# Kernel tuning notes

Hardware: AMD Instinct MI355X
Metric: run time of the kernel (lower is better)

Reference implementation:

```python
import jax, jax.numpy as jnp
import numpy as np

T_DIL = 10   # neighbor-count threshold
K_DIL = 2    # skip hyperparameter
BN_EPS = 1e-5
NORM_EPS = 1e-12


def _dilate_pattern(adj_bool, mask_b):
    """Sequential (row-by-row) dilated neighbor skipping on a [N,N] bool adjacency.
    Faithful to the torch double loop: earlier rows' removals (including the
    symmetric column zeroing) affect later rows' neighbor sets."""
    N = adj_bool.shape[0]

    def step(carry, n):
        row = jnp.take(carry, n, axis=0)                 # [N] bool, current neighbors of n
        nbi = row.astype(jnp.int32)
        num = jnp.sum(nbi)
        sf = jnp.where(num > T_DIL, (num + K_DIL - 1) // K_DIL, 1)  # linear mode, ceil(num/k)
        rank = jnp.cumsum(nbi)                           # 1-based rank among neighbors
        rm = row & ((rank % sf) == 0)                    # neighbors[sf-1::sf]
        valid = (mask_b[n] != 0) & (num > 1)
        rm = jnp.where(valid, rm, False)
        keep = ~rm
        carry = carry.at[n].set(row & keep)              # adj[n, to_remove] = 0
        carry = carry.at[:, n].set(carry[:, n] & keep)   # adj[to_remove, n] = 0
        return carry, None

    out, _ = jax.lax.scan(step, adj_bool, jnp.arange(N))
    return out


def _dilate(adj, mask):
    # keep-pattern is piecewise constant in adj; multiply so removed entries -> 0
    keep = jax.vmap(_dilate_pattern)(adj > 0, mask)
    return adj * keep.astype(adj.dtype)


def _sage(x, adj, Wr, Wx, b, mf):
    # DenseSAGEConv: mean-aggregate, lin_rel + lin_root, L2 normalize, mask
    deg = jnp.clip(jnp.sum(adj, axis=-1, keepdims=True), 1.0, None)
    agg = jnp.einsum('bij,bjd->bid', adj, x) / deg
    out = agg @ Wr + x @ Wx + b
    nrm = jnp.maximum(jnp.linalg.norm(out, axis=-1, keepdims=True), NORM_EPS)
    return (out / nrm) * mf[..., None]


def _bn(x, g, b):
    # BatchNorm1d in training mode over flattened (B*N) rows, biased variance
    m = jnp.mean(x, axis=(0, 1))
    v = jnp.var(x, axis=(0, 1))
    return (x - m) * jax.lax.rsqrt(v + BN_EPS) * g + b


def _forward(x, adj, mask, Wr1, Wx1, b1, g1, be1, Wr2, Wx2, b2, g2, be2,
             Wr3, Wx3, b3, g3, be3, Wl, bl):
    mf = mask.astype(x.dtype)
    # linear dilation mode: skip factor is layer-independent, and each layer
    # dilates the ORIGINAL adj (torch clones adj per call) -> compute once
    adj_d = _dilate(adj, mask)
    h1 = _bn(jax.nn.relu(_sage(x, adj_d, Wr1, Wx1, b1, mf)), g1, be1)
    h2 = _bn(jax.nn.relu(_sage(h1, adj_d, Wr2, Wx2, b2, mf)), g2, be2)
    h3 = _bn(jax.nn.relu(_sage(h2, adj_d, Wr3, Wx3, b3, mf)), g3, be3)
    xc = jnp.concatenate([h1, h2, h3], axis=-1) * mf[..., None]
    return (xc @ Wl + bl) * mf[..., None]


def setup_inputs() -> dict:
    B, N, D, H, E = 8, 2048, 128, 128, 128
    key = jax.random.key(0)
    ks = jax.random.split(key, 24)
    x = jax.random.normal(ks[0], (B, N, D), dtype=jnp.float32)
    a = jax.random.bernoulli(ks[1], 0.01, (B, N, N))
    a = a | jnp.swapaxes(a, 1, 2)
    a = a & ~jnp.eye(N, dtype=bool)[None]
    adj = a.astype(jnp.float32)
    mask = jnp.ones((B, N), dtype=jnp.int32)
    s = 0.05
    p = {}
    dims = [(D, H), (H, H), (H, E)]
    for i, (di, do) in enumerate(dims, 1):
        p[f'Wr{i}'] = s * jax.random.normal(ks[2 * i], (di, do), dtype=jnp.float32)
        p[f'Wx{i}'] = s * jax.random.normal(ks[2 * i + 1], (di, do), dtype=jnp.float32)
        p[f'b{i}'] = jnp.zeros((do,), dtype=jnp.float32)
        p[f'g{i}'] = jnp.ones((do,), dtype=jnp.float32)
        p[f'be{i}'] = jnp.zeros((do,), dtype=jnp.float32)
    p['Wl'] = s * jax.random.normal(ks[10], (2 * H + E, E), dtype=jnp.float32)
    p['bl'] = jnp.zeros((E,), dtype=jnp.float32)
    return {'x': x, 'adj': adj, 'mask': mask, **p}


def reference(x, adj, mask, Wr1, Wx1, b1, g1, be1, Wr2, Wx2, b2, g2, be2,
              Wr3, Wx3, b3, g3, be3, Wl, bl):
    return _forward(x, adj, mask, Wr1, Wx1, b1, g1, be1, Wr2, Wx2, b2, g2, be2,
                    Wr3, Wx3, b3, g3, be3, Wl, bl)
```

## Files before the change

kernel.cpp:

```cpp
#include <hip/hip_runtime.h>
#include <cstdint>

constexpr int B_ = 8, N_ = 2048, D_ = 128, NW = 64;
constexpr int EMAX = 131072;
constexpr int RPS = 2064;
constexpr int TDIL = 10;

constexpr size_t OFF_BITSET = 0;
constexpr size_t OFF_AGG    = 0;
constexpr size_t OFF_H1     = (size_t)8  << 20;
constexpr size_t OFF_H2     = (size_t)16 << 20;
constexpr size_t OFF_H3     = (size_t)24 << 20;
constexpr size_t OFF_COLS   = (size_t)32 << 20;
constexpr size_t OFF_PACKED = (size_t)34 << 20;
constexpr size_t OFF_RP     = (size_t)38 << 20;
constexpr size_t OFF_DEG0   = OFF_RP   + ((size_t)128 << 10);
constexpr size_t OFF_DEGF   = OFF_DEG0 + ((size_t)64  << 10);
constexpr size_t OFF_RMASK  = OFF_DEGF + ((size_t)64  << 10);
constexpr size_t OFF_BN     = OFF_RMASK + ((size_t)256 << 10);
constexpr size_t OFF_WHI    = OFF_BN  + ((size_t)4 << 10);
constexpr size_t OFF_WLO    = OFF_WHI + ((size_t)304 << 10);

typedef __attribute__((ext_vector_type(8))) short short8v;
typedef __attribute__((ext_vector_type(4))) float f32x4;

__global__ __launch_bounds__(256) void kW_prep(
        const float* __restrict__ Wr1, const float* __restrict__ Wx1,
        const float* __restrict__ Wr2, const float* __restrict__ Wx2,
        const float* __restrict__ Wr3, const float* __restrict__ Wx3,
        const float* __restrict__ Wl,
        uint16_t* __restrict__ whi, uint16_t* __restrict__ wlo,
        float* __restrict__ bn) {
    if (blockIdx.x == 0) {
        for (int i = threadIdx.x; i < 768; i += 256) bn[i] = 0.f;
    }
    int g  = blockIdx.x >> 5;
    int lb = blockIdx.x & 31;
    int K = (g == 3) ? 384 : 256;
    const float* A  = (g == 0) ? Wr1 : (g == 1) ? Wr2 : (g == 2) ? Wr3 : Wl;
    const float* Bw = (g == 0) ? Wx1 : (g == 1) ? Wx2 : (g == 2) ? Wx3 : nullptr;
    size_t base = (g == 3) ? (size_t)98304 : (size_t)g * 32768;
    int total = K * 128;
    for (int f = lb * 256 + threadIdx.x; f < total; f += 32 * 256) {
        int e = f & 7, lane = (f >> 3) & 63, ct = (f >> 9) & 7, ks = f >> 12;
        int k = ks * 32 + ((lane >> 4) << 3) + e;
        int col = (ct << 4) + (lane & 15);
        float v = (g == 3 || k < 128) ? A[(size_t)k * 128 + col]
                                      : Bw[(size_t)(k - 128) * 128 + col];
        uint32_t u = __float_as_uint(v);
        uint32_t hi = (u + 0x7FFFu + ((u >> 16) & 1u)) >> 16;
        float hf = __uint_as_float(hi << 16);
        uint32_t u2 = __float_as_uint(v - hf);
        uint32_t lo = (u2 + 0x7FFFu + ((u2 >> 16) & 1u)) >> 16;
        whi[base + f] = (uint16_t)hi;
        wlo[base + f] = (uint16_t)lo;
    }
}

__global__ __launch_bounds__(256) void k1_bitset(const float* __restrict__ adj,
        uint32_t* __restrict__ bitset, uint32_t* __restrict__ deg0) {
    int row  = blockIdx.x * 4 + (threadIdx.x >> 6);
    int lane = threadIdx.x & 63;
    const float* ar = adj + (size_t)row * N_;
    uint32_t myw = 0;
    #pragma unroll 4
    for (int it = 0; it < 32; ++it) {
        float v = ar[it * 64 + lane];
        unsigned long long m = __ballot(v != 0.0f);
        if (lane == 2 * it)          myw = (uint32_t)m;
        else if (lane == 2 * it + 1) myw = (uint32_t)(m >> 32);
    }
    bitset[(size_t)row * NW + lane] = myw;
    int pc = __popc(myw);
    #pragma unroll
    for (int off = 32; off >= 1; off >>= 1) pc += __shfl_xor(pc, off);
    if (lane == 0) deg0[row] = (uint32_t)pc;
}

__global__ __launch_bounds__(256) void k2_rowptr(const uint32_t* __restrict__ deg0,
        uint32_t* __restrict__ rowptr) {
    int b = blockIdx.x, t = threadIdx.x;
    __shared__ uint32_t tsum[256];
    uint32_t v[8]; uint32_t s = 0;
    #pragma unroll
    for (int j = 0; j < 8; ++j) { v[j] = deg0[b * N_ + t * 8 + j]; s += v[j]; v[j] = s; }
    tsum[t] = s;
    __syncthreads();
    for (int off = 1; off < 256; off <<= 1) {
        uint32_t xv = (t >= off) ? tsum[t - off] : 0u;
        __syncthreads();
        tsum[t] += xv;
        __syncthreads();
    }
    uint32_t excl = tsum[t] - s;
    uint32_t* rp = rowptr + (size_t)b * RPS;
    if (t == 0) rp[0] = 0;
    #pragma unroll
    for (int j = 0; j < 8; ++j) {
        uint32_t val = excl + v[j];
        if (val > (uint32_t)EMAX) val = EMAX;
        rp[t * 8 + j + 1] = val;
    }
}

__global__ __launch_bounds__(256) void k3_cols(const uint32_t* __restrict__ bitset,
        const uint32_t* __restrict__ rowptr, uint16_t* __restrict__ cols) {
    int row  = blockIdx.x * 4 + (threadIdx.x >> 6);
    int lane = threadIdx.x & 63;
    int b = row >> 11, n = row & (N_ - 1);
    uint32_t w = bitset[(size_t)row * NW + lane];
    uint32_t pc = __popc(w);
    uint32_t inc = pc;
    #pragma unroll
    for (int off = 1; off < 64; off <<= 1) {
        uint32_t t = __shfl_up(inc, off);
        if (lane >= off) inc += t;
    }
    uint32_t base = rowptr[(size_t)b * RPS + n] + (inc - pc);
    uint16_t* cb = cols + (size_t)b * EMAX;
    while (w) {
        int bit = __builtin_ctz(w); w &= w - 1;
        if (base < (uint32_t)EMAX) cb[base] = (uint16_t)(lane * 32 + bit);
        ++base;
    }
}

__global__ __launch_bounds__(256) void k4_packed(const uint16_t* __restrict__ cols,
        const uint32_t* __restrict__ rowptr, uint32_t* __restrict__ packed) {
    int row  = blockIdx.x * 4 + (threadIdx.x >> 6);
    int lane = threadIdx.x & 63;
    int b = row >> 11, n = row & (N_ - 1);
    const uint32_t* rpb = rowptr + (size_t)b * RPS;
    const uint16_t* cb  = cols + (size_t)b * EMAX;
    uint32_t start = rpb[n], end = rpb[n + 1];
    for (uint32_t e = start + lane; e < end; e += 64) {
        uint32_t j = cb[e];
        uint32_t lo = rpb[j], hi = rpb[j + 1];
        uint32_t rj = lo;
        while (lo < hi) {
            uint32_t mid = (lo + hi) >> 1;
            if ((int)cb[mid] < n) lo = mid + 1; else hi = mid;
        }
        packed[(size_t)b * EMAX + e] = j | ((lo - rj) << 16);
    }
}

#define K5_ISSUE(PK0, PK1, CNT, ROW)                                        \
    do {                                                                    \
        int rr_ = (ROW);                                                    \
        if (rr_ < N_) {                                                     \
            uint32_t ldI_ = rps[rr_], enI_ = rps[rr_ + 1];                  \
            CNT = (int)(enI_ - ldI_);                                       \
            PK0 = (lane < CNT)      ? pkg[ldI_ + lane]      : 0xFFFFFFFFu;  \
            PK1 = (lane + 64 < CNT) ? pkg[ldI_ + 64 + lane] : 0xFFFFFFFFu;  \
        } else { CNT = 0; PK0 = 0xFFFFFFFFu; PK1 = 0xFFFFFFFFu; }           \
    } while (0)

#define K5_PROC(PK0, PK1, CNT, NROW)                                        \
    do {                                                                    \
        int nr_ = (NROW);                                                   \
        uint32_t c0_ = PK0 & 0xFFFFu, c1_ = PK1 & 0xFFFFu;                  \
        bool e0_ = (lane < CNT)      && (c0_ < (uint32_t)nr_);              \
        bool e1_ = (lane + 64 < CNT) && (c1_ < (uint32_t)nr_);              \
        while (true) {                                                      \
            uint32_t d0_ = e0_ ? __hip_atomic_load(&done[c0_ >> 5],         \
                    __ATOMIC_ACQUIRE, __HIP_MEMORY_SCOPE_WORKGROUP) : 0u;   \
            uint32_t d1_ = e1_ ? __hip_atomic_load(&done[c1_ >> 5],         \
                    __ATOMIC_ACQUIRE, __HIP_MEMORY_SCOPE_WORKGROUP) : 0u;   \
            bool ok0_ = !e0_ || ((d0_ >> (c0_ & 31)) & 1u);                 \
            bool ok1_ = !e1_ || ((d1_ >> (c1_ & 31)) & 1u);                 \
            if (__all((int)(ok0_ && ok1_))) break;                          \
        }                                                                   \
        __builtin_amdgcn_s_setprio(1);                                      \
        uint4 mcur_ = *(const uint4*)&rm4[(size_t)nr_ * 4];                 \
        uint32_t w01_ = (lane < 32) ? mcur_.x : mcur_.y;                    \
        uint32_t w23_ = (lane < 32) ? mcur_.z : mcur_.w;                    \
        uint32_t a0_ = (w01_ >> (lane & 31)) & 1u;                          \
        uint32_t a1_ = (w23_ >> (lane & 31)) & 1u;                          \
        unsigned long long bl0_ = __ballot(a0_ != 0), bl1_ = __ballot(a1_ != 0); \
        uint32_t num_ = (uint32_t)__popcll(bl0_) + (uint32_t)__popcll(bl1_);\
        if (mk[nr_] && num_ > 1u) {                                         \
            bool allrm_ = num_ <= (uint32_t)TDIL;                           \
            uint32_t sf_ = (num_ + 1u) >> 1;                                \
            uint32_t r2_ = (num_ & 1u) ? 0xFFFFFFFFu : num_;                \
            uint32_t rank0_ = (uint32_t)__popcll(bl0_ & below) + 1u;        \
            uint32_t rank1_ = (uint32_t)__popcll(bl0_) +                    \
                              (uint32_t)__popcll(bl1_ & below) + 1u;        \
            bool rm0_ = a0_ && (allrm_ || rank0_ == sf_ || rank0_ == r2_);  \
            bool rm1_ = a1_ && (allrm_ || rank1_ == sf_ || rank1_ == r2_);  \
            unsigned long long rb0_ = __ballot(rm0_), rb1_ = __ballot(rm1_);\
            if (rm0_) {                                                     \
                uint32_t c_ = PK0 & 0xFFFFu, ml_ = PK0 >> 16;               \
                if (ml_ < 128u) atomicAnd(&rm4[c_ * 4 + (ml_ >> 5)], ~(1u << (ml_ & 31))); \
            }                                                               \
            if (rm1_) {                                                     \
                uint32_t c_ = PK1 & 0xFFFFu, ml_ = PK1 >> 16;               \
                if (ml_ < 128u) atomicAnd(&rm4[c_ * 4 + (ml_ >> 5)], ~(1u << (ml_ & 31))); \
            }                                                               \
            if (lane == 0) {                                                \
                uint4 nm_;                                                  \
                nm_.x = mcur_.x & ~(uint32_t)rb0_;                          \
                nm_.y = mcur_.y & ~(uint32_t)(rb0_ >> 32);                  \
                nm_.z = mcur_.z & ~(uint32_t)rb1_;                          \
                nm_.w = mcur_.w & ~(uint32_t)(rb1_ >> 32);                  \
                *(uint4*)&rm4[(size_t)nr_ * 4] = nm_;                       \
            }                                                               \
        }                                                                   \
        __asm__ __volatile__("" ::: "memory");                              \
        if (lane == 0)                                                      \
            __hip_atomic_fetch_or(&done[nr_ >> 5], 1u << (nr_ & 31),        \
                    __ATOMIC_RELAXED, __HIP_MEMORY_SCOPE_WORKGROUP);        \
        __builtin_amdgcn_s_setprio(0);                                      \
    } while (0)

__global__ __launch_bounds__(1024) void k5_dilate(
        const uint32_t* __restrict__ packed, const uint32_t* __restrict__ rowptr,
        const uint32_t* __restrict__ deg0, const int* __restrict__ mask,
        uint32_t* __restrict__ rmaskg, uint32_t* __restrict__ degf) {
    int b = blockIdx.x;
    int tid = threadIdx.x;
    int lane = tid & 63;
    int wv = tid >> 6;
    __shared__ __align__(16) uint32_t rm4[N_ * 4];
    __shared__ uint32_t rps[N_ + 1];
    __shared__ uint8_t  mk[N_];
    __shared__ uint32_t done[64];
    const uint32_t* pkg = packed + (size_t)b * EMAX;
    const uint32_t* rpg = rowptr + (size_t)b * RPS;

    for (int i = tid; i <= N_; i += 1024) rps[i] = rpg[i];
    if (tid < 64) done[tid] = 0u;
    for (int i = tid; i < N_; i += 1024) {
        int d = (int)deg0[b * N_ + i]; if (d > 128) d = 128;
        uint4 mm;
        mm.x = (d >= 32) ? ~0u : ((d > 0)  ? ((1u << d)        - 1u) : 0u);
        mm.y = (d >= 64) ? ~0u : ((d > 32) ? ((1u << (d - 32)) - 1u) : 0u);
        mm.z = (d >= 96) ? ~0u : ((d > 64) ? ((1u << (d - 64)) - 1u) : 0u);
        mm.w = (d >= 128)? ~0u : ((d > 96) ? ((1u << (d - 96)) - 1u) : 0u);
        *(uint4*)&rm4[(size_t)i * 4] = mm;
        mk[i] = (uint8_t)(mask[b * N_ + i] != 0);
    }
    __syncthreads();

    unsigned long long below = (1ULL << lane) - 1ULL;
    int cntA, cntB, cntC;
    uint32_t pkA0, pkA1, pkB0, pkB1, pkC0, pkC1;
    K5_ISSUE(pkA0, pkA1, cntA, wv);
    K5_ISSUE(pkB0, pkB1, cntB, wv + 16);
    K5_ISSUE(pkC0, pkC1, cntC, wv + 32);

    int n = wv;
    while (n < N_) {
        K5_PROC(pkA0, pkA1, cntA, n);
        K5_ISSUE(pkA0, pkA1, cntA, n + 48);
        n += 16; if (n >= N_) break;
        K5_PROC(pkB0, pkB1, cntB, n);
        K5_ISSUE(pkB0, pkB1, cntB, n + 48);
        n += 16; if (n >= N_) break;
        K5_PROC(pkC0, pkC1, cntC, n);
        K5_ISSUE(pkC0, pkC1, cntC, n + 48);
        n += 16;
    }
    __syncthreads();
    for (int i = tid; i < N_; i += 1024) {
        uint4 mm = *(const uint4*)&rm4[(size_t)i * 4];
        *(uint4*)&rmaskg[((size_t)b * N_ + i) * 4] = mm;
        degf[b * N_ + i] = (uint32_t)(__popc(mm.x) + __popc(mm.y) + __popc(mm.z) + __popc(mm.w));
    }
}

__global__ __launch_bounds__(256) void k6_compact(uint16_t* __restrict__ cols,
        const uint32_t* __restrict__ rowptr, const uint32_t* __restrict__ rmaskg) {
    int row  = blockIdx.x * 4 + (threadIdx.x >> 6);
    int lane = threadIdx.x & 63;
    int b = row >> 11, n = row & (N_ - 1);
    uint16_t* cb = cols + (size_t)b * EMAX;
    uint4 mm = *(const uint4*)&rmaskg[(size_t)row * 4];
    uint32_t st = rowptr[(size_t)b * RPS + n];
    uint32_t w01 = (lane < 32) ? mm.x : mm.y;
    uint32_t w23 = (lane < 32) ? mm.z : mm.w;
    uint32_t a0 = (w01 >> (lane & 31)) & 1u;
    uint32_t a1 = (w23 >> (lane & 31)) & 1u;
    unsigned long long b0 = __ballot(a0 != 0), b1 = __ballot(a1 != 0);
    unsigned long long below = (1ULL << lane) - 1ULL;
    uint16_t c0v = 0, c1v = 0;
    if (a0) c0v = cb[st + lane];
    if (a1) c1v = cb[st + 64 + lane];
    uint32_t i0 = st + (uint32_t)__popcll(b0 & below);
    uint32_t i1 = st + (uint32_t)__popcll(b0) + (uint32_t)__popcll(b1 & below);
    if (a0) cb[i0] = c0v;
    if (a1) cb[i1] = c1v;
}

__global__ __launch_bounds__(256) void k7_spmm(const float* __restrict__ X,
        const uint16_t* __restrict__ cols, const uint32_t* __restrict__ rowptr,
        const uint32_t* __restrict__ degf, float* __restrict__ agg) {
    int wid  = blockIdx.x * 4 + (threadIdx.x >> 6);
    int lane = threadIdx.x & 63;
    int b = wid >> 11, n = wid & (N_ - 1);
    const uint16_t* cb = cols + (size_t)b * EMAX;
    uint32_t start = rowptr[(size_t)b * RPS + n];
    uint32_t cnt = degf[wid];
    const float* Xb = X + ((size_t)b * N_) * D_;
    float ax = 0.f, ay = 0.f;
    for (uint32_t base = 0; base < cnt; base += 64) {
        int idx = (int)base + lane;
        int cl = (idx < (int)cnt) ? (int)cb[start + idx] : 0;
        int kmax = (int)cnt - (int)base; if (kmax > 64) kmax = 64;
        int k = 0;
        for (; k + 4 <= kmax; k += 4) {
            int cA = __shfl(cl, k),     cB = __shfl(cl, k + 1);
            int cC = __shfl(cl, k + 2), cD = __shfl(cl, k + 3);
            float2 vA = ((const float2*)(Xb + (size_t)cA * D_))[lane];
            float2 vB = ((const float2*)(Xb + (size_t)cB * D_))[lane];
            float2 vC = ((const float2*)(Xb + (size_t)cC * D_))[lane];
            float2 vD = ((const float2*)(Xb + (size_t)cD * D_))[lane];
            ax += vA.x + vB.x + vC.x + vD.x;
            ay += vA.y + vB.y + vC.y + vD.y;
        }
        for (; k < kmax; ++k) {
            int c = __shfl(cl, k);
            float2 v = ((const float2*)(Xb + (size_t)c * D_))[lane];
            ax += v.x; ay += v.y;
        }
    }
    float inv = 1.0f / (float)(cnt ? cnt : 1u);
    ((float2*)(agg + (size_t)wid * D_))[lane] = make_float2(ax * inv, ay * inv);
}

__device__ __forceinline__ void cvt_store4(uint16_t* hiA, uint16_t* loA,
                                           int idx, float4 v) {
    float vv[4] = {v.x, v.y, v.z, v.w};
    ushort4 hs, ls;
    uint16_t* hp = (uint16_t*)&hs; uint16_t* lp = (uint16_t*)&ls;
    #pragma unroll
    for (int i = 0; i < 4; ++i) {
        uint32_t u = __float_as_uint(vv[i]);
        uint32_t hi = (u + 0x7FFFu + ((u >> 16) & 1u)) >> 16;
        float hf = __uint_as_float(hi << 16);
        uint32_t u2 = __float_as_uint(vv[i] - hf);
        uint32_t lo = (u2 + 0x7FFFu + ((u2 >> 16) & 1u)) >> 16;
        hp[i] = (uint16_t)hi; lp[i] = (uint16_t)lo;
    }
    *(ushort4*)&hiA[idx] = hs;
    *(ushort4*)&loA[idx] = ls;
}

constexpr int ASTR = 264;
__global__ __launch_bounds__(256) void k8_mfma(const float* __restrict__ agg,
        const float* __restrict__ Hin,
        const uint16_t* __restrict__ whi, const uint16_t* __restrict__ wlo,
        const float* __restrict__ bias, const int* __restrict__ mask,
        const float* __restrict__ bnp, const float* __restrict__ gp,
        const float* __restrict__ bep, int use_bn,
        float* __restrict__ P, float* __restrict__ bnstat) {
    __shared__ __align__(16) char buf[2 * 32 * ASTR * 2];
    __shared__ float scL[128], shL[128];
    uint16_t* aHi = (uint16_t*)buf;
    uint16_t* aLo = (uint16_t*)(buf + 32 * ASTR * 2);
    float* outP = (float*)buf;
    int tid = threadIdx.x, lane = tid & 63, h = tid >> 6;
    size_t row0 = (size_t)blockIdx.x * 32;

    if (tid < 128) {
        float sc = 1.f, sh = 0.f;
        if (use_bn) {
            float mean = bnp[tid] * (1.f / 16384.f);
            float var  = bnp[128 + tid] * (1.f / 16384.f) - mean * mean;
            sc = gp[tid] * rsqrtf(var + 1e-5f);
            sh = bep[tid] - mean * sc;
        }
        scL[tid] = sc; shL[tid] = sh;
    }
    __syncthreads();

    for (int f = tid * 4; f < 4096; f += 1024) {
        int r = f >> 7, c = f & 127;
        float4 va = *(const float4*)&agg[(row0 + r) * 128 + c];
        float4 vx = *(const float4*)&Hin[(row0 + r) * 128 + c];
        float4 s4 = *(const float4*)&scL[c];
        float4 h4 = *(const float4*)&shL[c];
        va.x = va.x * s4.x + h4.x; va.y = va.y * s4.y + h4.y;
        va.z = va.z * s4.z + h4.z; va.w = va.w * s4.w + h4.w;
        vx.x = vx.x * s4.x + h4.x; vx.y = vx.y * s4.y + h4.y;
        vx.z = vx.z * s4.z + h4.z; vx.w = vx.w * s4.w + h4.w;
        cvt_store4(aHi, aLo, r * ASTR + c, va);
        cvt_store4(aHi, aLo, r * ASTR + 128 + c, vx);
    }
    __syncthreads();

    f32x4 acc00 = {0.f,0.f,0.f,0.f}, acc01 = acc00, acc10 = acc00, acc11 = acc00;
    int ct0 = h * 2, ct1 = h * 2 + 1;
    int arow = (lane & 15);
    int koff = (lane >> 4) * 8;
    #pragma unroll
    for (int ks = 0; ks < 8; ++ks) {
        int k0 = ks * 32 + koff;
        short8v a0h = *(short8v*)&aHi[arow * ASTR + k0];
        short8v a0l = *(short8v*)&aLo[arow * ASTR + k0];
        short8v a1h = *(short8v*)&aHi[(arow + 16) * ASTR + k0];
        short8v a1l = *(short8v*)&aLo[(arow + 16) * ASTR + k0];
        short8v b0h = *(const short8v*)&whi[(size_t)(((ks * 8 + ct0) << 6) + lane) * 8];
        short8v b0l = *(const short8v*)&wlo[(size_t)(((ks * 8 + ct0) << 6) + lane) * 8];
        short8v b1h = *(const short8v*)&whi[(size_t)(((ks * 8 + ct1) << 6) + lane) * 8];
        short8v b1l = *(const short8v*)&wlo[(size_t)(((ks * 8 + ct1) << 6) + lane) * 8];
        acc00 = __builtin_amdgcn_mfma_f32_16x16x32_bf16(a0h, b0h, acc00, 0, 0, 0);
        acc00 = __builtin_amdgcn_mfma_f32_16x16x32_bf16(a0h, b0l, acc00, 0, 0, 0);
        acc00 = __builtin_amdgcn_mfma_f32_16x16x32_bf16(a0l, b0h, acc00, 0, 0, 0);
        acc01 = __builtin_amdgcn_mfma_f32_16x16x32_bf16(a0h, b1h, acc01, 0, 0, 0);
        acc01 = __builtin_amdgcn_mfma_f32_16x16x32_bf16(a0h, b1l, acc01, 0, 0, 0);
        acc01 = __builtin_amdgcn_mfma_f32_16x16x32_bf16(a0l, b1h, acc01, 0, 0, 0);
        acc10 = __builtin_amdgcn_mfma_f32_16x16x32_bf16(a1h, b0h, acc10, 0, 0, 0);
        acc10 = __builtin_amdgcn_mfma_f32_16x16x32_bf16(a1h, b0l, acc10, 0, 0, 0);
        acc10 = __builtin_amdgcn_mfma_f32_16x16x32_bf16(a1l, b0h, acc10, 0, 0, 0);
        acc11 = __builtin_amdgcn_mfma_f32_16x16x32_bf16(a1h, b1h, acc11, 0, 0, 0);
        acc11 = __builtin_amdgcn_mfma_f32_16x16x32_bf16(a1h, b1l, acc11, 0, 0, 0);
        acc11 = __builtin_amdgcn_mfma_f32_16x16x32_bf16(a1l, b1h, acc11, 0, 0, 0);
    }
    __syncthreads();

    int orow = (lane >> 4) * 4;
    int oc0 = ct0 * 16 + (lane & 15);
    int oc1 = ct1 * 16 + (lane & 15);
    #pragma unroll
    for (int j = 0; j < 4; ++j) {
        outP[(orow + j) * 128 + oc0]      = acc00[j];
        outP[(orow + j) * 128 + oc1]      = acc01[j];
        outP[(16 + orow + j) * 128 + oc0] = acc10[j];
        outP[(16 + orow + j) * 128 + oc1] = acc11[j];
    }
    __syncthreads();

    float bs0 = bias[lane], bs1 = bias[lane + 64];
    #pragma unroll
    for (int i = 0; i < 8; ++i) {
        int r = h * 8 + i;
        float v0 = outP[r * 128 + lane] + bs0;
        float v1 = outP[r * 128 + lane + 64] + bs1;
        float s = v0 * v0 + v1 * v1;
        #pragma unroll
        for (int off = 32; off >= 1; off >>= 1) s += __shfl_xor(s, off);
        float nrm = fmaxf(sqrtf(s), 1e-12f);
        float mf = (mask[row0 + r] != 0) ? 1.f : 0.f;
        float inv = mf / nrm;
        float p0 = fmaxf(v0 * inv, 0.f), p1 = fmaxf(v1 * inv, 0.f);
        P[(row0 + r) * 128 + lane]      = p0;
        P[(row0 + r) * 128 + lane + 64] = p1;
        outP[r * 128 + lane] = p0; outP[r * 128 + lane + 64] = p1;
    }
    __syncthreads();
    if (tid < 128) {
        float s = 0.f, q = 0.f;
        #pragma unroll
        for (int r = 0; r < 32; ++r) { float v = outP[r * 128 + tid]; s += v; q += v * v; }
        atomicAdd(&bnstat[tid], s);
        atomicAdd(&bnstat[128 + tid], q);
    }
}

__global__ __launch_bounds__(256) void k11_final(const float* __restrict__ h1,
        const float* __restrict__ h2, const float* __restrict__ h3,
        const float* __restrict__ Wl, const float* __restrict__ bl,
        const int* __restrict__ mask, const float* __restrict__ bn,
        const float* __restrict__ g1, const float* __restrict__ be1,
        const float* __restrict__ g2, const float* __restrict__ be2,
        const float* __restrict__ g3, const float* __restrict__ be3,
        float* __restrict__ out) {
    __shared__ float s1[32 * 128], s2[32 * 128], s3[32 * 128];
    __shared__ float scA[128], shA[128], scB[128], shB[128], scC[128], shC[128];
    int tid = threadIdx.x;
    size_t row0 = (size_t)blockIdx.x * 32;
    if (tid < 128) {
        float m1 = bn[tid] * (1.f / 16384.f);
        float v1 = bn[128 + tid] * (1.f / 16384.f) - m1 * m1;
        scA[tid] = g1[tid] * rsqrtf(v1 + 1e-5f);
        shA[tid] = be1[tid] - m1 * scA[tid];
        float m2 = bn[256 + tid] * (1.f / 16384.f);
        float v2 = bn[384 + tid] * (1.f / 16384.f) - m2 * m2;
        scB[tid] = g2[tid] * rsqrtf(v2 + 1e-5f);
        shB[tid] = be2[tid] - m2 * scB[tid];
        float m3 = bn[512 + tid] * (1.f / 16384.f);
        float v3 = bn[640 + tid] * (1.f / 16384.f) - m3 * m3;
        scC[tid] = g3[tid] * rsqrtf(v3 + 1e-5f);
        shC[tid] = be3[tid] - m3 * scC[tid];
    }
    __syncthreads();
    for (int t = tid * 4; t < 32 * 128; t += 1024) {
        int r = t >> 7;
        float mf = (mask[row0 + r] != 0) ? 1.f : 0.f;
        int c = t & 127;
        float4 a = *(const float4*)&h1[row0 * 128 + t];
        float4 b = *(const float4*)&h2[row0 * 128 + t];
        float4 cc = *(const float4*)&h3[row0 * 128 + t];
        float4 sa = *(const float4*)&scA[c], ha = *(const float4*)&shA[c];
        float4 sb = *(const float4*)&scB[c], hb = *(const float4*)&shB[c];
        float4 sc = *(const float4*)&scC[c], hc = *(const float4*)&shC[c];
        a.x = (a.x * sa.x + ha.x) * mf; a.y = (a.y * sa.y + ha.y) * mf;
        a.z = (a.z * sa.z + ha.z) * mf; a.w = (a.w * sa.w + ha.w) * mf;
        b.x = (b.x * sb.x + hb.x) * mf; b.y = (b.y * sb.y + hb.y) * mf;
        b.z = (b.z * sb.z + hb.z) * mf; b.w = (b.w * sb.w + hb.w) * mf;
        cc.x = (cc.x * sc.x + hc.x) * mf; cc.y = (cc.y * sc.y + hc.y) * mf;
        cc.z = (cc.z * sc.z + hc.z) * mf; cc.w = (cc.w * sc.w + hc.w) * mf;
        *(float4*)&s1[t] = a; *(float4*)&s2[t] = b; *(float4*)&s3[t] = cc;
    }
    __syncthreads();
    int h = tid >> 6, c0 = (tid & 63) * 2;
    float2 acc[8];
    #pragma unroll
    for (int i = 0; i < 8; ++i) acc[i] = make_float2(0.f, 0.f);
    for (int k4 = 0; k4 < 128; k4 += 4) {
        float2 w1[4], w2[4], w3[4];
        #pragma unroll
        for (int kk = 0; kk < 4; ++kk) {
            w1[kk] = *(const float2*)&Wl[(k4 + kk) * 128 + c0];
            w2[kk] = *(const float2*)&Wl[(128 + k4 + kk) * 128 + c0];
            w3[kk] = *(const float2*)&Wl[(256 + k4 + kk) * 128 + c0];
        }
        #pragma unroll
        for (int i = 0; i < 8; ++i) {
            int r = h * 8 + i;
            float4 a = *(const float4*)&s1[r * 128 + k4];
            float4 b = *(const float4*)&s2[r * 128 + k4];
            float4 c = *(const float4*)&s3[r * 128 + k4];
            acc[i].x += a.x * w1[0].x + a.y * w1[1].x + a.z * w1[2].x + a.w * w1[3].x
                      + b.x * w2[0].x + b.y * w2[1].x + b.z * w2[2].x + b.w * w2[3].x
                      + c.x * w3[0].x + c.y * w3[1].x + c.z * w3[2].x + c.w * w3[3].x;
            acc[i].y += a.x * w1[0].y + a.y * w1[1].y + a.z * w1[2].y + a.w * w1[3].y
                      + b.x * w2[0].y + b.y * w2[1].y + b.z * w2[2].y + b.w * w2[3].y
                      + c.x * w3[0].y + c.y * w3[1].y + c.z * w3[2].y + c.w * w3[3].y;
        }
    }
    float bx = bl[c0], by = bl[c0 + 1];
    #pragma unroll
    for (int i = 0; i < 8; ++i) {
        int r = h * 8 + i;
        float mf = (mask[row0 + r] != 0) ? 1.f : 0.f;
        *(float2*)&out[(row0 + r) * 128 + c0] =
            make_float2((acc[i].x + bx) * mf, (acc[i].y + by) * mf);
    }
}

extern "C" void kernel_launch(void* const* d_in, const int* in_sizes, int n_in,
                              void* d_out, int out_size, void* d_ws, size_t ws_size,
                              hipStream_t stream) {
    (void)in_sizes; (void)n_in; (void)out_size; (void)ws_size;
    const float* x    = (const float*)d_in[0];
    const float* adj  = (const float*)d_in[1];
    const int*   mask = (const int*)d_in[2];
    const float* Wr1 = (const float*)d_in[3],  *Wx1 = (const float*)d_in[4];
    const float* b1  = (const float*)d_in[5],  *g1  = (const float*)d_in[6],  *be1 = (const float*)d_in[7];
    const float* Wr2 = (const float*)d_in[8],  *Wx2 = (const float*)d_in[9];
    const float* b2  = (const float*)d_in[10], *g2  = (const float*)d_in[11], *be2 = (const float*)d_in[12];
    const float* Wr3 = (const float*)d_in[13], *Wx3 = (const float*)d_in[14];
    const float* b3  = (const float*)d_in[15], *g3  = (const float*)d_in[16], *be3 = (const float*)d_in[17];
    const float* Wl  = (const float*)d_in[18], *bl  = (const float*)d_in[19];

    char* ws = (char*)d_ws;
    uint32_t* bitset = (uint32_t*)(ws + OFF_BITSET);
    float*    agg    = (float*)(ws + OFF_AGG);
    float*    h1     = (float*)(ws + OFF_H1);
    float*    h2     = (float*)(ws + OFF_H2);
    float*    h3     = (float*)(ws + OFF_H3);
    uint16_t* cols   = (uint16_t*)(ws + OFF_COLS);
    uint32_t* packed = (uint32_t*)(ws + OFF_PACKED);
    uint32_t* rp     = (uint32_t*)(ws + OFF_RP);
    uint32_t* deg0   = (uint32_t*)(ws + OFF_DEG0);
    uint32_t* degf   = (uint32_t*)(ws + OFF_DEGF);
    uint32_t* rmaskg = (uint32_t*)(ws + OFF_RMASK);
    float*    bn     = (float*)(ws + OFF_BN);
    uint16_t* whi    = (uint16_t*)(ws + OFF_WHI);
    uint16_t* wlo    = (uint16_t*)(ws + OFF_WLO);
    float*    out    = (float*)d_out;

    kW_prep   <<<128,  256, 0, stream>>>(Wr1, Wx1, Wr2, Wx2, Wr3, Wx3, Wl, whi, wlo, bn);
    k1_bitset <<<4096, 256, 0, stream>>>(adj, bitset, deg0);
    k2_rowptr <<<8,    256, 0, stream>>>(deg0, rp);
    k3_cols   <<<4096, 256, 0, stream>>>(bitset, rp, cols);
    k4_packed <<<4096, 256, 0, stream>>>(cols, rp, packed);
    k5_dilate <<<8,    1024, 0, stream>>>(packed, rp, deg0, mask, rmaskg, degf);
    k6_compact<<<4096, 256, 0, stream>>>(cols, rp, rmaskg);
    k7_spmm   <<<4096, 256, 0, stream>>>(x,  cols, rp, degf, agg);
    k8_mfma   <<<512,  256, 0, stream>>>(agg, x,  whi,          wlo,          b1, mask,
                                         bn, g1, be1, 0, h1, bn + 0);
    k7_spmm   <<<4096, 256, 0, stream>>>(h1, cols, rp, degf, agg);
    k8_mfma   <<<512,  256, 0, stream>>>(agg, h1, whi + 32768,  wlo + 32768,  b2, mask,
                                         bn + 0, g1, be1, 1, h2, bn + 256);
    k7_spmm   <<<4096, 256, 0, stream>>>(h2, cols, rp, degf, agg);
    k8_mfma   <<<512,  256, 0, stream>>>(agg, h2, whi + 65536,  wlo + 65536,  b3, mask,
                                         bn + 256, g2, be2, 1, h3, bn + 512);
    k11_final <<<512,  256, 0, stream>>>(h1, h2, h3, Wl, bl, mask, bn,
                                         g1, be1, g2, be2, g3, be3, out);
}
```

Measured before the change: 325.1 us.

## Fuse dilation with compaction and overlap layer-1 root GEMM on idle CUs

The sequential dilation kernel, which uses only 8 blocks, now also runs 512 extra blocks that compute the layer-1 root term x@Wx1+b1 with MFMA on otherwise idle CUs, so layer 1's k8 only does the aggregate half of K. Column compaction is folded into the dilation kernel, which removes the k6 launch and the global rmask round trip. The dependency tracking changes from atomic bitmask words to per-row byte flags, with a barrier after each 16-row generation so each wave waits only on rows inside the current generation. This adds shared-memory aliasing, reuses the h3 buffer for the xwx term, and relies on the barrier and volatile byte flags to keep the sequential order correct.

```diff
diff --git a/kernel.cpp b/kernel.cpp
--- a/kernel.cpp
+++ b/kernel.cpp
@@ -16,8 +16,7 @@
 constexpr size_t OFF_RP     = (size_t)38 << 20;
 constexpr size_t OFF_DEG0   = OFF_RP   + ((size_t)128 << 10);
 constexpr size_t OFF_DEGF   = OFF_DEG0 + ((size_t)64  << 10);
-constexpr size_t OFF_RMASK  = OFF_DEGF + ((size_t)64  << 10);
-constexpr size_t OFF_BN     = OFF_RMASK + ((size_t)256 << 10);
+constexpr size_t OFF_BN     = OFF_DEGF + ((size_t)64  << 10);
 constexpr size_t OFF_WHI    = OFF_BN  + ((size_t)4 << 10);
 constexpr size_t OFF_WLO    = OFF_WHI + ((size_t)304 << 10);
 
@@ -145,6 +144,10 @@
     }
 }
 
+#define GEN_SYNC() do {                                                     \
+        __asm__ __volatile__("s_waitcnt lgkmcnt(0)" ::: "memory");          \
+        __builtin_amdgcn_s_barrier(); } while (0)
+
 #define K5_ISSUE(PK0, PK1, CNT, ROW)                                        \
     do {                                                                    \
         int rr_ = (ROW);                                                    \
@@ -159,43 +162,48 @@
 #define K5_PROC(PK0, PK1, CNT, NROW)                                        \
     do {                                                                    \
         int nr_ = (NROW);                                                   \
+        uint32_t gb_ = (uint32_t)(nr_ - wv);                                \
+        bool two_ = (CNT > 64);                                             \
         uint32_t c0_ = PK0 & 0xFFFFu, c1_ = PK1 & 0xFFFFu;                  \
-        bool e0_ = (lane < CNT)      && (c0_ < (uint32_t)nr_);              \
-        bool e1_ = (lane + 64 < CNT) && (c1_ < (uint32_t)nr_);              \
+        bool e0_ = (lane < CNT) && (c0_ >= gb_) && (c0_ < (uint32_t)nr_);   \
+        bool e1_ = two_ && (lane + 64 < CNT) && (c1_ >= gb_) && (c1_ < (uint32_t)nr_); \
         while (true) {                                                      \
-            uint32_t d0_ = e0_ ? __hip_atomic_load(&done[c0_ >> 5],         \
-                    __ATOMIC_ACQUIRE, __HIP_MEMORY_SCOPE_WORKGROUP) : 0u;   \
-            uint32_t d1_ = e1_ ? __hip_atomic_load(&done[c1_ >> 5],         \
-                    __ATOMIC_ACQUIRE, __HIP_MEMORY_SCOPE_WORKGROUP) : 0u;   \
-            bool ok0_ = !e0_ || ((d0_ >> (c0_ & 31)) & 1u);                 \
-            bool ok1_ = !e1_ || ((d1_ >> (c1_ & 31)) & 1u);                 \
-            if (__all((int)(ok0_ && ok1_))) break;                          \
+            uint32_t d0_ = e0_ ? *(volatile uint8_t*)&doneB[c0_] : 1u;      \
+            uint32_t d1_ = e1_ ? *(volatile uint8_t*)&doneB[c1_] : 1u;      \
+            if (__all((int)((d0_ != 0u) & (d1_ != 0u)))) break;             \
         }                                                                   \
-        __builtin_amdgcn_s_setprio(1);                                      \
         uint4 mcur_ = *(const uint4*)&rm4[(size_t)nr_ * 4];                 \
         uint32_t w01_ = (lane < 32) ? mcur_.x : mcur_.y;                    \
-        uint32_t w23_ = (lane < 32) ? mcur_.z : mcur_.w;                    \
         uint32_t a0_ = (w01_ >> (lane & 31)) & 1u;                          \
-        uint32_t a1_ = (w23_ >> (lane & 31)) & 1u;                          \
-        unsigned long long bl0_ = __ballot(a0_ != 0), bl1_ = __ballot(a1_ != 0); \
+        unsigned long long bl0_ = __ballot(a0_ != 0);                       \
+        uint32_t a1_ = 0; unsigned long long bl1_ = 0;                      \
+        if (two_) {                                                         \
+            uint32_t w23_ = (lane < 32) ? mcur_.z : mcur_.w;                \
+            a1_ = (w23_ >> (lane & 31)) & 1u;                               \
+            bl1_ = __ballot(a1_ != 0);                                      \
+        }                                                                   \
         uint32_t num_ = (uint32_t)__popcll(bl0_) + (uint32_t)__popcll(bl1_);\
         if (mk[nr_] && num_ > 1u) {                                         \
             bool allrm_ = num_ <= (uint32_t)TDIL;                           \
             uint32_t sf_ = (num_ + 1u) >> 1;                                \
             uint32_t r2_ = (num_ & 1u) ? 0xFFFFFFFFu : num_;                \
             uint32_t rank0_ = (uint32_t)__popcll(bl0_ & below) + 1u;        \
-            uint32_t rank1_ = (uint32_t)__popcll(bl0_) +                    \
-                              (uint32_t)__popcll(bl1_ & below) + 1u;        \
             bool rm0_ = a0_ && (allrm_ || rank0_ == sf_ || rank0_ == r2_);  \
-            bool rm1_ = a1_ && (allrm_ || rank1_ == sf_ || rank1_ == r2_);  \
-            unsigned long long rb0_ = __ballot(rm0_), rb1_ = __ballot(rm1_);\
+            unsigned long long rb0_ = __ballot(rm0_);                       \
+            unsigned long long rb1_ = 0;                                    \
             if (rm0_) {                                                     \
-                uint32_t c_ = PK0 & 0xFFFFu, ml_ = PK0 >> 16;               \
-                if (ml_ < 128u) atomicAnd(&rm4[c_ * 4 + (ml_ >> 5)], ~(1u << (ml_ & 31))); \
+                uint32_t ml_ = PK0 >> 16;                                   \
+                if (ml_ < 128u) atomicAnd(&rm4[c0_ * 4 + (ml_ >> 5)], ~(1u << (ml_ & 31))); \
             }                                                               \
-            if (rm1_) {                                                     \
-                uint32_t c_ = PK1 & 0xFFFFu, ml_ = PK1 >> 16;               \
-                if (ml_ < 128u) atomicAnd(&rm4[c_ * 4 + (ml_ >> 5)], ~(1u << (ml_ & 31))); \
+            if (two_) {                                                     \
+                uint32_t rank1_ = (uint32_t)__popcll(bl0_) +                \
+                                  (uint32_t)__popcll(bl1_ & below) + 1u;    \
+                bool rm1_ = a1_ && (allrm_ || rank1_ == sf_ || rank1_ == r2_); \
+                rb1_ = __ballot(rm1_);                                      \
+                if (rm1_) {                                                 \
+                    uint32_t ml_ = PK1 >> 16;                               \
+                    if (ml_ < 128u) atomicAnd(&rm4[c1_ * 4 + (ml_ >> 5)], ~(1u << (ml_ & 31))); \
+                }                                                           \
             }                                                               \
             if (lane == 0) {                                                \
                 uint4 nm_;                                                  \
@@ -207,29 +215,81 @@
             }                                                               \
         }                                                                   \
         __asm__ __volatile__("" ::: "memory");                              \
-        if (lane == 0)                                                      \
-            __hip_atomic_fetch_or(&done[nr_ >> 5], 1u << (nr_ & 31),        \
-                    __ATOMIC_RELAXED, __HIP_MEMORY_SCOPE_WORKGROUP);        \
-        __builtin_amdgcn_s_setprio(0);                                      \
+        if (lane == 0) *(volatile uint8_t*)&doneB[nr_] = 1u;                \
     } while (0)
 
-__global__ __launch_bounds__(1024) void k5_dilate(
+constexpr int XSTR = 136;
+__global__ __launch_bounds__(1024) void k5_fused(
         const uint32_t* __restrict__ packed, const uint32_t* __restrict__ rowptr,
         const uint32_t* __restrict__ deg0, const int* __restrict__ mask,
-        uint32_t* __restrict__ rmaskg, uint32_t* __restrict__ degf) {
-    int b = blockIdx.x;
+        uint16_t* __restrict__ cols, uint32_t* __restrict__ degf,
+        const float* __restrict__ x, const uint16_t* __restrict__ whi,
+        const uint16_t* __restrict__ wlo, const float* __restrict__ b1,
+        float* __restrict__ xwx) {
+    __shared__ __align__(16) char sbuf[45060];
     int tid = threadIdx.x;
     int lane = tid & 63;
+
+    if (blockIdx.x >= 8) {
+        uint16_t* xHi = (uint16_t*)sbuf;
+        uint16_t* xLo = (uint16_t*)(sbuf + 32 * XSTR * 2);
+        size_t row0 = (size_t)(blockIdx.x - 8) * 32;
+        {
+            int f = tid * 4;
+            int r = f >> 7, c = f & 127;
+            float4 v = *(const float4*)&x[(row0 + r) * 128 + c];
+            float vv[4] = {v.x, v.y, v.z, v.w};
+            ushort4 hs, ls;
+            uint16_t* hp = (uint16_t*)&hs; uint16_t* lp = (uint16_t*)&ls;
+            #pragma unroll
+            for (int i = 0; i < 4; ++i) {
+                uint32_t u = __float_as_uint(vv[i]);
+                uint32_t hi = (u + 0x7FFFu + ((u >> 16) & 1u)) >> 16;
+                float hf = __uint_as_float(hi << 16);
+                uint32_t u2 = __float_as_uint(vv[i] - hf);
+                uint32_t lo = (u2 + 0x7FFFu + ((u2 >> 16) & 1u)) >> 16;
+                hp[i] = (uint16_t)hi; lp[i] = (uint16_t)lo;
+            }
+            *(ushort4*)&xHi[r * XSTR + c] = hs;
+            *(ushort4*)&xLo[r * XSTR + c] = ls;
+        }
+        __syncthreads();
+        int h = tid >> 6;
+        int rt = h >> 3, ct = h & 7;
+        int arow = rt * 16 + (lane & 15);
+        int koff = (lane >> 4) * 8;
+        f32x4 acc = {0.f, 0.f, 0.f, 0.f};
+        #pragma unroll
+        for (int ks = 0; ks < 4; ++ks) {
+            short8v ah = *(short8v*)&xHi[arow * XSTR + ks * 32 + koff];
+            short8v al = *(short8v*)&xLo[arow * XSTR + ks * 32 + koff];
+            size_t bi = (size_t)((((ks + 4) * 8 + ct) << 6) + lane) * 8;
+            short8v bh = *(const short8v*)&whi[bi];
+            short8v bl = *(const short8v*)&wlo[bi];
+            acc = __builtin_amdgcn_mfma_f32_16x16x32_bf16(ah, bh, acc, 0, 0, 0);
+            acc = __builtin_amdgcn_mfma_f32_16x16x32_bf16(ah, bl, acc, 0, 0, 0);
+            acc = __builtin_amdgcn_mfma_f32_16x16x32_bf16(al, bh, acc, 0, 0, 0);
+        }
+        int oc = ct * 16 + (lane & 15);
+        int orow = rt * 16 + (lane >> 4) * 4;
+        float bb = b1[oc];
+        #pragma unroll
+        for (int j = 0; j < 4; ++j)
+            xwx[(row0 + orow + j) * 128 + oc] = acc[j] + bb;
+        return;
+    }
+
+    int b = blockIdx.x;
     int wv = tid >> 6;
-    __shared__ __align__(16) uint32_t rm4[N_ * 4];
-    __shared__ uint32_t rps[N_ + 1];
-    __shared__ uint8_t  mk[N_];
-    __shared__ uint32_t done[64];
+    uint32_t* rm4   = (uint32_t*)sbuf;
+    uint32_t* rps   = (uint32_t*)(sbuf + 32768);
+    uint8_t*  mk    = (uint8_t*)(sbuf + 32768 + 8196);
+    uint8_t*  doneB = mk + 2048;
     const uint32_t* pkg = packed + (size_t)b * EMAX;
     const uint32_t* rpg = rowptr + (size_t)b * RPS;
+    uint16_t* cbm = cols + (size_t)b * EMAX;
 
     for (int i = tid; i <= N_; i += 1024) rps[i] = rpg[i];
-    if (tid < 64) done[tid] = 0u;
     for (int i = tid; i < N_; i += 1024) {
         int d = (int)deg0[b * N_ + i]; if (d > 128) d = 128;
         uint4 mm;
@@ -239,6 +299,7 @@
         mm.w = (d >= 128)? ~0u : ((d > 96) ? ((1u << (d - 96)) - 1u) : 0u);
         *(uint4*)&rm4[(size_t)i * 4] = mm;
         mk[i] = (uint8_t)(mask[b * N_ + i] != 0);
+        doneB[i] = 0;
     }
     __syncthreads();
 
@@ -253,43 +314,38 @@
     while (n < N_) {
         K5_PROC(pkA0, pkA1, cntA, n);
         K5_ISSUE(pkA0, pkA1, cntA, n + 48);
+        GEN_SYNC();
         n += 16; if (n >= N_) break;
         K5_PROC(pkB0, pkB1, cntB, n);
         K5_ISSUE(pkB0, pkB1, cntB, n + 48);
+        GEN_SYNC();
         n += 16; if (n >= N_) break;
         K5_PROC(pkC0, pkC1, cntC, n);
         K5_ISSUE(pkC0, pkC1, cntC, n + 48);
+        GEN_SYNC();
         n += 16;
     }
     __syncthreads();
-    for (int i = tid; i < N_; i += 1024) {
+
+    for (int i = wv; i < N_; i += 16) {
         uint4 mm = *(const uint4*)&rm4[(size_t)i * 4];
-        *(uint4*)&rmaskg[((size_t)b * N_ + i) * 4] = mm;
-        degf[b * N_ + i] = (uint32_t)(__popc(mm.x) + __popc(mm.y) + __popc(mm.z) + __popc(mm.w));
-    }
-}
-
-__global__ __launch_bounds__(256) void k6_compact(uint16_t* __restrict__ cols,
-        const uint32_t* __restrict__ rowptr, const uint32_t* __restrict__ rmaskg) {
-    int row  = blockIdx.x * 4 + (threadIdx.x >> 6);
-    int lane = threadIdx.x & 63;
-    int b = row >> 11, n = row & (N_ - 1);
-    uint16_t* cb = cols + (size_t)b * EMAX;
-    uint4 mm = *(const uint4*)&rmaskg[(size_t)row * 4];
-    uint32_t st = rowptr[(size_t)b * RPS + n];
-    uint32_t w01 = (lane < 32) ? mm.x : mm.y;
-    uint32_t w23 = (lane < 32) ? mm.z : mm.w;
-    uint32_t a0 = (w01 >> (lane & 31)) & 1u;
-    uint32_t a1 = (w23 >> (lane & 31)) & 1u;
-    unsigned long long b0 = __ballot(a0 != 0), b1 = __ballot(a1 != 0);
-    unsigned long long below = (1ULL << lane) - 1ULL;
-    uint16_t c0v = 0, c1v = 0;
-    if (a0) c0v = cb[st + lane];
-    if (a1) c1v = cb[st + 64 + lane];
-    uint32_t i0 = st + (uint32_t)__popcll(b0 & below);
-    uint32_t i1 = st + (uint32_t)__popcll(b0) + (uint32_t)__popcll(b1 & below);
-    if (a0) cb[i0] = c0v;
-    if (a1) cb[i1] = c1v;
+        if (lane == 0)
+            degf[b * N_ + i] = (uint32_t)(__popc(mm.x) + __popc(mm.y) +
+                                          __popc(mm.z) + __popc(mm.w));
+        uint32_t st = rps[i];
+        uint32_t w01 = (lane < 32) ? mm.x : mm.y;
+        uint32_t w23 = (lane < 32) ? mm.z : mm.w;
+        uint32_t a0 = (w01 >> (lane & 31)) & 1u;
+        uint32_t a1 = (w23 >> (lane & 31)) & 1u;
+        unsigned long long b0 = __ballot(a0 != 0), b1v = __ballot(a1 != 0);
+        uint16_t c0v = 0, c1v = 0;
+        if (a0) c0v = cbm[st + lane];
+        if (a1) c1v = cbm[st + 64 + lane];
+        uint32_t i0 = st + (uint32_t)__popcll(b0 & below);
+        uint32_t i1 = st + (uint32_t)__popcll(b0) + (uint32_t)__popcll(b1v & below);
+        if (a0) cbm[i0] = c0v;
+        if (a1) cbm[i1] = c1v;
+    }
 }
 
 __global__ __launch_bounds__(256) void k7_spmm(const float* __restrict__ X,
@@ -353,6 +409,7 @@
         const float* __restrict__ bias, const int* __restrict__ mask,
         const float* __restrict__ bnp, const float* __restrict__ gp,
         const float* __restrict__ bep, int use_bn,
+        const float* __restrict__ xwx,
         float* __restrict__ P, float* __restrict__ bnstat) {
     __shared__ __align__(16) char buf[2 * 32 * ASTR * 2];
     __shared__ float scL[128], shL[128];
@@ -377,24 +434,28 @@
     for (int f = tid * 4; f < 4096; f += 1024) {
         int r = f >> 7, c = f & 127;
         float4 va = *(const float4*)&agg[(row0 + r) * 128 + c];
-        float4 vx = *(const float4*)&Hin[(row0 + r) * 128 + c];
         float4 s4 = *(const float4*)&scL[c];
         float4 h4 = *(const float4*)&shL[c];
         va.x = va.x * s4.x + h4.x; va.y = va.y * s4.y + h4.y;
         va.z = va.z * s4.z + h4.z; va.w = va.w * s4.w + h4.w;
-        vx.x = vx.x * s4.x + h4.x; vx.y = vx.y * s4.y + h4.y;
-        vx.z = vx.z * s4.z + h4.z; vx.w = vx.w * s4.w + h4.w;
         cvt_store4(aHi, aLo, r * ASTR + c, va);
-        cvt_store4(aHi, aLo, r * ASTR + 128 + c, vx);
-    }
-    __syncthreads();
-
+        if (!xwx) {
+            float4 vx = *(const float4*)&Hin[(row0 + r) * 128 + c];
+            vx.x = vx.x * s4.x + h4.x; vx.y = vx.y * s4.y + h4.y;
+            vx.z = vx.z * s4.z + h4.z; vx.w = vx.w * s4.w + h4.w;
+            cvt_store4(aHi, aLo, r * ASTR + 128 + c, vx);
+        }
+    }
+    __syncthreads();
+
+    int ksN = xwx ? 4 : 8;
     f32x4 acc00 = {0.f,0.f,0.f,0.f}, acc01 = acc00, acc10 = acc00, acc11 = acc00;
     int ct0 = h * 2, ct1 = h * 2 + 1;
     int arow = (lane & 15);
     int koff = (lane >> 4) * 8;
     #pragma unroll
     for (int ks = 0; ks < 8; ++ks) {
+        if (ks >= ksN) continue;
         int k0 = ks * 32 + koff;
         short8v a0h = *(short8v*)&aHi[arow * ASTR + k0];
         short8v a0l = *(short8v*)&aLo[arow * ASTR + k0];
@@ -435,8 +496,10 @@
     #pragma unroll
     for (int i = 0; i < 8; ++i) {
         int r = h * 8 + i;
-        float v0 = outP[r * 128 + lane] + bs0;
-        float v1 = outP[r * 128 + lane + 64] + bs1;
+        float ad0 = xwx ? xwx[(row0 + r) * 128 + lane]      : bs0;
+        float ad1 = xwx ? xwx[(row0 + r) * 128 + lane + 64] : bs1;
+        float v0 = outP[r * 128 + lane] + ad0;
+        float v1 = outP[r * 128 + lane + 64] + ad1;
         float s = v0 * v0 + v1 * v1;
         #pragma unroll
         for (int off = 32; off >= 1; off >>= 1) s += __shfl_xor(s, off);
@@ -561,12 +624,12 @@
     float*    h1     = (float*)(ws + OFF_H1);
     float*    h2     = (float*)(ws + OFF_H2);
     float*    h3     = (float*)(ws + OFF_H3);
+    float*    xwx    = (float*)(ws + OFF_H3);
     uint16_t* cols   = (uint16_t*)(ws + OFF_COLS);
     uint32_t* packed = (uint32_t*)(ws + OFF_PACKED);
     uint32_t* rp     = (uint32_t*)(ws + OFF_RP);
     uint32_t* deg0   = (uint32_t*)(ws + OFF_DEG0);
     uint32_t* degf   = (uint32_t*)(ws + OFF_DEGF);
-    uint32_t* rmaskg = (uint32_t*)(ws + OFF_RMASK);
     float*    bn     = (float*)(ws + OFF_BN);
     uint16_t* whi    = (uint16_t*)(ws + OFF_WHI);
     uint16_t* wlo    = (uint16_t*)(ws + OFF_WLO);
@@ -577,17 +640,17 @@
     k2_rowptr <<<8,    256, 0, stream>>>(deg0, rp);
     k3_cols   <<<4096, 256, 0, stream>>>(bitset, rp, cols);
     k4_packed <<<4096, 256, 0, stream>>>(cols, rp, packed);
-    k5_dilate <<<8,    1024, 0, stream>>>(packed, rp, deg0, mask, rmaskg, degf);
-    k6_compact<<<4096, 256, 0, stream>>>(cols, rp, rmaskg);
+    k5_fused  <<<520,  1024, 0, stream>>>(packed, rp, deg0, mask, cols, degf,
+                                          x, whi, wlo, b1, xwx);
     k7_spmm   <<<4096, 256, 0, stream>>>(x,  cols, rp, degf, agg);
-    k8_mfma   <<<512,  256, 0, stream>>>(agg, x,  whi,          wlo,          b1, mask,
-                                         bn, g1, be1, 0, h1, bn + 0);
+    k8_mfma   <<<512,  256, 0, stream>>>(agg, x,  whi,         wlo,         b1, mask,
+                                         bn, g1, be1, 0, xwx, h1, bn + 0);
     k7_spmm   <<<4096, 256, 0, stream>>>(h1, cols, rp, degf, agg);
-    k8_mfma   <<<512,  256, 0, stream>>>(agg, h1, whi + 32768,  wlo + 32768,  b2, mask,
-                                         bn + 0, g1, be1, 1, h2, bn + 256);
+    k8_mfma   <<<512,  256, 0, stream>>>(agg, h1, whi + 32768, wlo + 32768, b2, mask,
+                                         bn + 0, g1, be1, 1, nullptr, h2, bn + 256);
     k7_spmm   <<<4096, 256, 0, stream>>>(h2, cols, rp, degf, agg);
-    k8_mfma   <<<512,  256, 0, stream>>>(agg, h2, whi + 65536,  wlo + 65536,  b3, mask,
-                                         bn + 256, g2, be2, 1, h3, bn + 512);
+    k8_mfma   <<<512,  256, 0, stream>>>(agg, h2, whi + 65536, wlo + 65536, b3, mask,
+                                         bn + 256, g2, be2, 1, nullptr, h3, bn + 512);
     k11_final <<<512,  256, 0, stream>>>(h1, h2, h3, Wl, bl, mask, bn,
                                          g1, be1, g2, be2, g3, be3, out);
 }
```

Result: slower. 410.0 us (+26.1%).
